# Optimization experiments

Hardware: AMD Instinct MI355X
Metric: run time of the kernel (lower is better)

Reference implementation:

```python
import jax, jax.numpy as jnp
import numpy as np

B = 16
L = 3
INNER = 96
EXPAND = 2 * INNER
NC = 80
C_INS = [128, 256, 512]
HWS = [(80, 80), (40, 40), (20, 20)]
STRIDES = [8, 16, 32]
PRIOR = 0.01


def _conv(x, w, b, groups=1, pad=0):
    # x: [B,Cin,H,W], w: [Cout,Cin//groups,kh,kw]
    y = jax.lax.conv_general_dilated(
        x, w, window_strides=(1, 1), padding=[(pad, pad), (pad, pad)],
        feature_group_count=groups)
    return y + b[None, :, None, None]


def _inverted_residual(x, w1, b1, wd, bd, w2, b2):
    # 1x1 expand -> SiLU -> 3x3 depthwise -> SiLU -> 1x1 project, residual (stride 1, cin==cout)
    y = jax.nn.silu(_conv(x, w1, b1))
    y = jax.nn.silu(_conv(y, wd, bd, groups=w1.shape[0], pad=1))
    y = _conv(y, w2, b2)
    return x + y


def setup_inputs() -> dict:
    key = jax.random.key(0)
    keys = iter(jax.random.split(key, 64))

    def nrm(shape, s=0.03):
        return jax.random.normal(next(keys), shape, jnp.float32) * s

    d = {}
    for k in range(L):
        h, w = HWS[k]
        d[f"x{k}"] = jax.random.normal(next(keys), (B, C_INS[k], h, w), jnp.float32)
        d[f"stem_w{k}"] = nrm((INNER, C_INS[k], 1, 1))
        d[f"stem_b{k}"] = jnp.zeros((INNER,), jnp.float32)
    for p in ("cls", "reg"):
        d[p + "_w1"] = nrm((L, EXPAND, INNER, 1, 1))
        d[p + "_b1"] = jnp.zeros((L, EXPAND), jnp.float32)
        d[p + "_wd"] = nrm((L, EXPAND, 1, 3, 3))
        d[p + "_bd"] = jnp.zeros((L, EXPAND), jnp.float32)
        d[p + "_w2"] = nrm((L, INNER, EXPAND, 1, 1))
        d[p + "_b2"] = jnp.zeros((L, INNER), jnp.float32)
    bias_init = float(-np.log((1.0 - PRIOR) / PRIOR))
    d["clsp_w"] = nrm((L, NC, INNER, 1, 1))
    d["clsp_b"] = jnp.full((L, NC), bias_init, jnp.float32)
    d["regp_w"] = nrm((L, 4, INNER, 1, 1))
    d["regp_b"] = jnp.zeros((L, 4), jnp.float32)
    d["objp_w"] = nrm((L, 1, INNER, 1, 1))
    d["objp_b"] = jnp.full((L, 1), bias_init, jnp.float32)
    return d


def _forward(xs, params):
    outs = []
    for k in range(L):
        x = jax.nn.silu(_conv(xs[k], params[f"stem_w{k}"], params[f"stem_b{k}"]))  # CBR stem
        cls_feat = _inverted_residual(
            x, params["cls_w1"][k], params["cls_b1"][k], params["cls_wd"][k],
            params["cls_bd"][k], params["cls_w2"][k], params["cls_b2"][k])
        reg_feat = _inverted_residual(
            x, params["reg_w1"][k], params["reg_b1"][k], params["reg_wd"][k],
            params["reg_bd"][k], params["reg_w2"][k], params["reg_b2"][k])
        cls_out = _conv(cls_feat, params["clsp_w"][k], params["clsp_b"][k])  # [B,NC,H,W]
        reg_out = _conv(reg_feat, params["regp_w"][k], params["regp_b"][k])  # [B,4,H,W]
        obj_out = _conv(reg_feat, params["objp_w"][k], params["objp_b"][k])  # [B,1,H,W]
        h, w = HWS[k]
        yv, xv = jnp.meshgrid(jnp.arange(h, dtype=jnp.float32),
                              jnp.arange(w, dtype=jnp.float32), indexing="ij")
        grid = jnp.stack((xv, yv), 0)[None]  # [1,2,H,W]
        s = float(STRIDES[k])
        o = jnp.concatenate([
            (reg_out[:, :2] + grid) * s,
            jnp.exp(reg_out[:, 2:4]) * s,
            jax.nn.sigmoid(obj_out),
            jax.nn.sigmoid(cls_out),
        ], axis=1)  # [B, 5+NC, H, W]
        outs.append(o.reshape(B, 5 + NC, h * w).transpose(0, 2, 1))
    return jnp.concatenate(outs, axis=1)  # [B, 8400, 5+NC]


def reference(x0, x1, x2,
              stem_w0, stem_b0, stem_w1, stem_b1, stem_w2, stem_b2,
              cls_w1, cls_b1, cls_wd, cls_bd, cls_w2, cls_b2,
              reg_w1, reg_b1, reg_wd, reg_bd, reg_w2, reg_b2,
              clsp_w, clsp_b, regp_w, regp_b, objp_w, objp_b):
    params = dict(stem_w0=stem_w0, stem_b0=stem_b0, stem_w1=stem_w1, stem_b1=stem_b1,
                  stem_w2=stem_w2, stem_b2=stem_b2,
                  cls_w1=cls_w1, cls_b1=cls_b1, cls_wd=cls_wd, cls_bd=cls_bd,
                  cls_w2=cls_w2, cls_b2=cls_b2,
                  reg_w1=reg_w1, reg_b1=reg_b1, reg_wd=reg_wd, reg_bd=reg_bd,
                  reg_w2=reg_w2, reg_b2=reg_b2,
                  clsp_w=clsp_w, clsp_b=clsp_b, regp_w=regp_w, regp_b=regp_b,
                  objp_w=objp_w, objp_b=objp_b)
    return _forward([x0, x1, x2], params)
```

## Files before the change

### kernel.cpp

```cpp
#include <hip/hip_runtime.h>

typedef unsigned int uint32;
using half2v  = __attribute__((ext_vector_type(2))) _Float16;
using half4v  = __attribute__((ext_vector_type(4))) _Float16;
using half8   = __attribute__((ext_vector_type(8))) _Float16;
using floatx4 = __attribute__((ext_vector_type(4))) float;

__device__ __forceinline__ float sigm_f(float x){
  return __builtin_amdgcn_rcpf(1.0f + __expf(-x));
}
__device__ __forceinline__ float silu_f(float x){ return x * sigm_f(x); }

__device__ __forceinline__ half2v pkrtz(float a, float b){
  return __builtin_bit_cast(half2v, __builtin_amdgcn_cvt_pkrtz(a, b));
}

__device__ __forceinline__ void gll16(const _Float16* src, _Float16* ldsDst){
  __builtin_amdgcn_global_load_lds(
      (const __attribute__((address_space(1))) uint32*)src,
      (__attribute__((address_space(3))) uint32*)ldsDst, 16, 0, 0);
}

#define OFF_W2    196608
#define OFF_HEAD  307200
#define OFF_WDT   330240
#define OFF_ROBJ  340608
#define OFF_DWB   345216
#define WTOT      346368

#define PPOS 143552L
#define EXPAD_ELEMS 27561984L
#define NDW  134400L

__global__ __launch_bounds__(256) void wconv_k(
    const float* __restrict__ s0, const float* __restrict__ s1,
    const float* __restrict__ s2, const float* __restrict__ cw1,
    const float* __restrict__ rw1, const float* __restrict__ cw2,
    const float* __restrict__ rw2, const float* __restrict__ chw,
    const float* __restrict__ cwd, const float* __restrict__ rwd,
    const float* __restrict__ rpw, const float* __restrict__ opw,
    const float* __restrict__ cbd, const float* __restrict__ rbd,
    _Float16* __restrict__ dst)
{
  int i = blockIdx.x*256 + threadIdx.x;
  if (i >= WTOT) return;
  float v;
  if (i < OFF_WDT) {
    const float* p; int off;
    if      (i < 12288)  { p = s0;  off = i; }
    else if (i < 36864)  { p = s1;  off = i - 12288; }
    else if (i < 86016)  { p = s2;  off = i - 36864; }
    else if (i < 141312) { p = cw1; off = i - 86016; }
    else if (i < 196608) { p = rw1; off = i - 141312; }
    else if (i < 251904) { p = cw2; off = i - 196608; }
    else if (i < 307200) { p = rw2; off = i - 251904; }
    else                 { p = chw; off = i - 307200; }
    v = p[off];
  } else if (i < OFF_ROBJ) {
    int rel = i - OFF_WDT;
    int br = rel / 5184; int r2 = rel - br*5184;
    int lvl = r2 / 1728; int r3 = r2 - lvl*1728;
    int j = r3 / 192;    int c = r3 - j*192;
    const float* wd = br ? rwd : cwd;
    v = wd[lvl*1728 + c*9 + j];
  } else if (i < OFF_DWB) {
    int rel = i - OFF_ROBJ;
    int lvl = rel / 1536; int r2 = rel - lvl*1536;
    int co = r2 / 96;     int k = r2 - co*96;
    v = (co < 4) ? rpw[lvl*384 + co*96 + k] : (co == 4 ? opw[lvl*96 + k] : 0.f);
  } else {
    int rel = i - OFF_DWB;
    int br = rel / 576;  int r2 = rel - br*576;
    int lvl = r2 / 192;  int c = r2 - lvl*192;
    v = (br ? rbd : cbd)[lvl*192 + c];
  }
  dst[i] = (_Float16)v;
}

__global__ __launch_bounds__(256) void zpad_k(_Float16* __restrict__ exBase)
{
  int ci = blockIdx.x*256 + threadIdx.x;
  if (ci >= 439296) return;
  int br = ci / 219648; int r = ci - br*219648;
  int W, PLB, rem, perimg;
  if (r < 124416)      { W=80; PLB=0;      rem = r;          perimg = 7776; }
  else if (r < 187392) { W=40; PLB=107584; rem = r - 124416; perimg = 3936; }
  else                 { W=20; PLB=135808; rem = r - 187392; perimg = 2016; }
  int b = rem / perimg; int t3 = rem - b*perimg;
  int p = t3 / 24; int g = t3 - p*24;
  int PW = W + 2;
  int row, col;
  if (p < 2*PW) { row = (p >= PW) ? (W+1) : 0; col = (p >= PW) ? (p - PW) : p; }
  else { int q = p - 2*PW; row = 1 + (q >> 1); col = (q & 1) ? (W+1) : 0; }
  long pp = (long)PLB + (long)b*PW*PW + row*PW + col;
  half8 z = {(_Float16)0,(_Float16)0,(_Float16)0,(_Float16)0,
             (_Float16)0,(_Float16)0,(_Float16)0,(_Float16)0};
  *(half8*)(exBase + br*EXPAD_ELEMS + ((long)g*PPOS + pp)*8) = z;
}

__global__ __launch_bounds__(256) void stem_k(
    const float* __restrict__ x0, const float* __restrict__ x1,
    const float* __restrict__ x2, const _Float16* __restrict__ Wb,
    const float* __restrict__ sb0, const float* __restrict__ sb1,
    const float* __restrict__ sb2, _Float16* __restrict__ Out)
{
  const int m0 = blockIdx.x << 7;
  const int lvl = (m0 < 102400) ? 0 : (m0 < 128000 ? 1 : 2);
  const int CIN = (lvl==0)?128:(lvl==1?256:512);
  const int HW  = (lvl==0)?6400:(lvl==1?1600:400);
  const int noff= (lvl==0)?0:(lvl==1?102400:128000);
  const float* X = (lvl==0)?x0:(lvl==1?x1:x2);
  const _Float16* Wl = Wb + ((lvl==0)?0:(lvl==1?12288:36864));
  const float* bias = (lvl==0)?sb0:(lvl==1?sb1:sb2);

  int t=threadIdx.x, lane=t&63, wv=t>>6, mr=lane&15, quad=lane>>4;

  int idx[2];
  #pragma unroll
  for (int nt=0; nt<2; ++nt) {
    int n = m0 + wv*32 + nt*16 + mr;
    int m = n - noff; int b_ = m / HW; int p = m - b_*HW;
    idx[nt] = (b_*CIN + quad*8)*HW + p;
  }
  const _Float16* Ap = Wl + mr*CIN + quad*8;

  floatx4 zero = {0.f,0.f,0.f,0.f};
  floatx4 acc[6][2];
  #pragma unroll
  for (int i=0;i<6;++i)
    #pragma unroll
    for (int j=0;j<2;++j) acc[i][j] = zero;

  for (int k=0; k<CIN; k+=32) {
    half8 a[6], b[2];
    #pragma unroll
    for (int mt=0; mt<6; ++mt) a[mt] = *(const half8*)(Ap + mt*16*CIN);
    #pragma unroll
    for (int nt=0; nt<2; ++nt) {
      float f[8];
      #pragma unroll
      for (int j=0;j<8;++j) f[j] = X[idx[nt] + j*HW];
      half2v* bh = (half2v*)&b[nt];
      #pragma unroll
      for (int j=0;j<4;++j) bh[j] = pkrtz(f[2*j], f[2*j+1]);
    }
    #pragma unroll
    for (int mt=0; mt<6; ++mt)
      #pragma unroll
      for (int nt=0; nt<2; ++nt)
        acc[mt][nt] = __builtin_amdgcn_mfma_f32_16x16x32_f16(a[mt], b[nt], acc[mt][nt], 0, 0, 0);
    Ap += 32;
    #pragma unroll
    for (int nt=0; nt<2; ++nt) idx[nt] += 32*HW;
  }

  #pragma unroll
  for (int mt=0; mt<6; ++mt) {
    float4 bv = *(const float4*)(bias + mt*16 + quad*4);
    int co = mt*16 + quad*4;
    int g = co >> 3; int h = co & 7;
    #pragma unroll
    for (int nt=0; nt<2; ++nt) {
      int pos = m0 + wv*32 + nt*16 + mr;
      half4v o;
      o[0] = (_Float16)silu_f(acc[mt][nt][0] + bv.x);
      o[1] = (_Float16)silu_f(acc[mt][nt][1] + bv.y);
      o[2] = (_Float16)silu_f(acc[mt][nt][2] + bv.z);
      o[3] = (_Float16)silu_f(acc[mt][nt][3] + bv.w);
      *(half4v*)(Out + ((long)g*NDW + pos)*8 + h) = o;
    }
  }
}

__global__ __launch_bounds__(256) void expand2_k(
    const _Float16* __restrict__ A, const _Float16* __restrict__ wbf,
    const float* __restrict__ b1c, const float* __restrict__ b1r,
    _Float16* __restrict__ OutBase)
{
  const int bz = blockIdx.z;
  const _Float16* Wb = wbf + 86016 + bz*55296;
  _Float16* Out = OutBase + bz*EXPAD_ELEMS;
  const float* b1 = bz ? b1r : b1c;

  int orig = blockIdx.x;
  int xcd = orig & 7; int loc = orig >> 3;
  int bx = (xcd < 2 ? xcd*132 : 2*132 + (xcd-2)*131) + loc;

  const int m0 = bx << 7;
  const int lvl = (m0 < 102400) ? 0 : (m0 < 128000 ? 1 : 2);
  const int HW  = (lvl==0)?6400:(lvl==1?1600:400);
  const int W   = (lvl==0)?80:(lvl==1?40:20);
  const int noff= (lvl==0)?0:(lvl==1?102400:128000);
  const int PLB = (lvl==0)?0:(lvl==1?107584:135808);
  const int PW  = W + 2;
  const int co0 = blockIdx.y * 96;
  int t = threadIdx.x, lane = t & 63, wv = t >> 6;
  int mr = lane & 15, quad = lane >> 4;
  const _Float16* Ap0 = A + ((long)quad*NDW + (m0 + wv*32 + mr))*8;
  const _Float16* Bp = Wb + ((long)(co0 + mr))*96 + quad*8;
  const float* bp = b1 + lvl*192 + co0;

  floatx4 zero = {0.f,0.f,0.f,0.f};
  floatx4 acc[6][2];
  #pragma unroll
  for (int i=0;i<6;++i)
    #pragma unroll
    for (int j=0;j<2;++j) acc[i][j] = zero;

  #pragma unroll
  for (int k=0; k<3; ++k) {
    half8 wf[6], af[2];
    #pragma unroll
    for (int mt=0; mt<6; ++mt) wf[mt] = *(const half8*)(Bp + (long)mt*16*96);
    #pragma unroll
    for (int nt=0; nt<2; ++nt)
      af[nt] = *(const half8*)(Ap0 + ((long)k*4*NDW)*8 + nt*16*8);
    #pragma unroll
    for (int mt=0; mt<6; ++mt)
      #pragma unroll
      for (int nt=0; nt<2; ++nt)
        acc[mt][nt] = __builtin_amdgcn_mfma_f32_16x16x32_f16(wf[mt], af[nt], acc[mt][nt], 0, 0, 0);
    Bp += 32;
  }

  long pp2[2];
  #pragma unroll
  for (int nt=0; nt<2; ++nt) {
    int gm = m0 + wv*32 + nt*16 + mr;
    int m = gm - noff; int b_ = m / HW; int rp = m - b_*HW;
    int y = rp / W;  int x = rp - y*W;
    pp2[nt] = PLB + ((long)b_*PW + (y+1))*PW + (x+1);
  }

  #pragma unroll
  for (int mt=0; mt<6; ++mt) {
    float4 bv = *(const float4*)(bp + mt*16 + quad*4);
    int co = co0 + mt*16 + quad*4;
    int g = co >> 3;
    int h = (co & 4);
    #pragma unroll
    for (int nt=0; nt<2; ++nt) {
      half4v o;
      o[0] = (_Float16)silu_f(acc[mt][nt][0] + bv.x);
      o[1] = (_Float16)silu_f(acc[mt][nt][1] + bv.y);
      o[2] = (_Float16)silu_f(acc[mt][nt][2] + bv.z);
      o[3] = (_Float16)silu_f(acc[mt][nt][3] + bv.w);
      *(half4v*)(Out + ((long)g*PPOS + pp2[nt])*8 + h) = o;
    }
  }
}

#define PSTRIDE 104
__global__ __launch_bounds__(256, 3) void dwprojhead_k(
    const _Float16* __restrict__ exBase, const _Float16* __restrict__ wbf,
    const float* __restrict__ b2_c, const float* __restrict__ b2_r,
    const _Float16* __restrict__ resid,
    const float* __restrict__ hb, const float* __restrict__ rb,
    const float* __restrict__ ob, float* __restrict__ out)
{
  __shared__ _Float16 halo[24*800];
  __shared__ _Float16 ldsP[64*PSTRIDE];
  const int bz = blockIdx.y;
  const _Float16* ex = exBase + bz*EXPAD_ELEMS;
  const float* b2 = bz ? b2_r : b2_c;

  int orig = blockIdx.x;
  int bx = (orig & 7)*268 + (orig >> 3);

  int lvl, W, HW, noff, a0, PLB;
  int b_, y0, x0;
  if (bx < 1600) {
    lvl = 0; W = 80; HW = 6400; noff = 0;      a0 = 0;    PLB = 0;
    b_ = bx / 100; int tl = bx - b_*100;
    y0 = (tl / 10) * 8; x0 = (tl - (tl/10)*10) * 8;
  } else if (bx < 2000) {
    lvl = 1; W = 40; HW = 1600; noff = 102400; a0 = 6400; PLB = 107584;
    int rel = bx - 1600; b_ = rel / 25; int tl = rel - b_*25;
    y0 = (tl / 5) * 8; x0 = (tl - (tl/5)*5) * 8;
  } else {
    lvl = 2; W = 20; HW = 400; noff = 128000; a0 = 8000; PLB = 135808;
    int rel = bx - 2000; b_ = rel / 9; int tl = rel - b_*9;
    int iy = tl / 3; int ix = tl - iy*3;
    y0 = iy*6; x0 = ix*6;
  }
  const int PW = W + 2;

  int t = threadIdx.x, lane = t & 63, wv = t >> 6;
  int mr = lane & 15, quad = lane >> 4;
  const int p = wv*16 + mr;

  const _Float16* wT = wbf + OFF_WDT + bz*5184 + lvl*1728;
  const _Float16* bB = wbf + OFF_DWB + bz*576 + lvl*192;
  const _Float16* Ap = wbf + OFF_W2 + bz*55296 + lvl*18432 + ((long)mr)*192 + quad*8;

  const int n = noff + b_*HW + (y0 + (p>>3))*W + x0 + (p&7);

  floatx4 pacc[6];
  {
    floatx4 zero = {0.f,0.f,0.f,0.f};
    #pragma unroll
    for (int j=0;j<6;++j) pacc[j] = zero;
  }

  half4v rsv[6];

  const long pb00 = (long)PLB + ((long)b_*PW + y0)*PW + x0;
  {
    int e1 = lane;
    int hy1 = e1 / 10, hx1 = e1 - hy1*10;
    long s1 = pb00 + hy1*PW + hx1;
    int e2 = 64 + lane;
    int hy2 = e2 / 10, hx2 = e2 - hy2*10;
    long s2 = pb00 + hy2*PW + hx2;
    #pragma unroll
    for (int j = 0; j < 6; ++j) {
      int g = wv*6 + j;
      gll16(ex + ((long)g*PPOS + s1)*8, halo + g*800);
      if (lane < 36)
        gll16(ex + ((long)g*PPOS + s2)*8, halo + g*800 + 512);
    }
  }
  #pragma unroll
  for (int mt=0; mt<6; ++mt) {
    int co = mt*16 + quad*4;
    int g = co >> 3; int h = co & 7;
    rsv[mt] = *(const half4v*)(resid + ((long)g*NDW + n)*8 + h);
  }
  __syncthreads();

  {
    const int ty = p >> 3, tx = p & 7;
    const _Float16* hb0 = halo + (ty*10 + tx)*8;
    for (int k = 0; k < 6; ++k) {
      const int g = 4*k + quad;
      const _Float16* hg = hb0 + g*800;
      const _Float16* wp = wT + g*8;

      half8 a[9], w[9];
      #pragma unroll
      for (int dy = 0; dy < 3; ++dy)
        #pragma unroll
        for (int dx = 0; dx < 3; ++dx)
          a[dy*3+dx] = *(const half8*)(hg + (dy*10 + dx)*8);
      #pragma unroll
      for (int tap = 0; tap < 9; ++tap)
        w[tap] = *(const half8*)(wp + tap*192);
      half8 bv8 = *(const half8*)(bB + g*8);
      half8 wf[6];
      #pragma unroll
      for (int mt = 0; mt < 6; ++mt)
        wf[mt] = *(const half8*)(Ap + (long)mt*16*192 + k*32);

      half2v ac0 = {bv8[0], bv8[1]};
      half2v ac1 = {bv8[2], bv8[3]};
      half2v ac2 = {bv8[4], bv8[5]};
      half2v ac3 = {bv8[6], bv8[7]};
      #pragma unroll
      for (int tap = 0; tap < 9; ++tap) {
        ac0 += half2v{a[tap][0],a[tap][1]} * half2v{w[tap][0],w[tap][1]};
        ac1 += half2v{a[tap][2],a[tap][3]} * half2v{w[tap][2],w[tap][3]};
        ac2 += half2v{a[tap][4],a[tap][5]} * half2v{w[tap][4],w[tap][5]};
        ac3 += half2v{a[tap][6],a[tap][7]} * half2v{w[tap][6],w[tap][7]};
      }
      half8 af;
      {
        half2v* oh = (half2v*)&af;
        oh[0] = pkrtz(silu_f((float)ac0[0]), silu_f((float)ac0[1]));
        oh[1] = pkrtz(silu_f((float)ac1[0]), silu_f((float)ac1[1]));
        oh[2] = pkrtz(silu_f((float)ac2[0]), silu_f((float)ac2[1]));
        oh[3] = pkrtz(silu_f((float)ac3[0]), silu_f((float)ac3[1]));
      }
      #pragma unroll
      for (int mt = 0; mt < 6; ++mt)
        pacc[mt] = __builtin_amdgcn_mfma_f32_16x16x32_f16(wf[mt], af, pacc[mt], 0, 0, 0);
    }
  }

  {
    const float* bp2 = b2 + lvl*96;
    #pragma unroll
    for (int mt=0; mt<6; ++mt) {
      int co = mt*16 + quad*4;
      float4 bv = *(const float4*)(bp2 + co);
      half4v o;
      o[0] = (_Float16)(pacc[mt][0] + bv.x + (float)rsv[mt][0]);
      o[1] = (_Float16)(pacc[mt][1] + bv.y + (float)rsv[mt][1]);
      o[2] = (_Float16)(pacc[mt][2] + bv.z + (float)rsv[mt][2]);
      o[3] = (_Float16)(pacc[mt][3] + bv.w + (float)rsv[mt][3]);
      *(half4v*)(ldsP + p*PSTRIDE + co) = o;
    }
  }

  if (bz == 0) {
    const _Float16* Bp = wbf + OFF_HEAD + lvl*7680 + ((long)mr)*96 + quad*8;
    const float* bp = hb + lvl*80;
    floatx4 zero = {0.f,0.f,0.f,0.f};
    floatx4 acc[5];
    #pragma unroll
    for (int j=0;j<5;++j) acc[j] = zero;

    #pragma unroll
    for (int k=0; k<3; ++k) {
      half8 a = *(const half8*)(ldsP + (wv*16 + mr)*PSTRIDE + k*32 + quad*8);
      half8 b[5];
      #pragma unroll
      for (int nt=0; nt<5; ++nt)
        b[nt] = *(const half8*)(Bp + (long)nt*16*96 + k*32);
      #pragma unroll
      for (int nt=0; nt<5; ++nt)
        acc[nt] = __builtin_amdgcn_mfma_f32_16x16x32_f16(a, b[nt], acc[nt], 0, 0, 0);
    }

    #pragma unroll
    for (int nt=0; nt<5; ++nt) {
      int co = nt*16 + mr;
      float bv = bp[co];
      #pragma unroll
      for (int r=0; r<4; ++r) {
        int pq = wv*16 + quad*4 + r;
        int rpp = (y0 + (pq>>3))*W + x0 + (pq&7);
        out[((long)(b_*8400 + a0 + rpp))*85 + 5 + co] = sigm_f(acc[nt][r] + bv);
      }
    }
  } else {
    const _Float16* Bp = wbf + OFF_ROBJ + lvl*1536 + ((long)mr)*96 + quad*8;
    float bv = (mr < 4) ? rb[lvl*4 + mr] : ((mr == 4) ? ob[lvl] : 0.f);
    float sc = (lvl==0) ? 8.f : (lvl==1 ? 16.f : 32.f);
    floatx4 acc = {0.f,0.f,0.f,0.f};
    #pragma unroll
    for (int k=0; k<3; ++k) {
      half8 a = *(const half8*)(ldsP + (wv*16 + mr)*PSTRIDE + k*32 + quad*8);
      half8 b = *(const half8*)(Bp + k*32);
      acc = __builtin_amdgcn_mfma_f32_16x16x32_f16(a, b, acc, 0, 0, 0);
    }
    #pragma unroll
    for (int r=0; r<4; ++r) {
      int pq = wv*16 + quad*4 + r;
      int yy = y0 + (pq>>3); int xx = x0 + (pq&7);
      int rpp = yy*W + xx;
      float v = acc[r] + bv;
      float o;
      if      (mr == 0) o = (v + (float)xx)*sc;
      else if (mr == 1) o = (v + (float)yy)*sc;
      else if (mr <  4) o = __expf(v)*sc;
      else              o = sigm_f(v);
      if (mr < 5)
        out[((long)(b_*8400 + a0 + rpp))*85 + mr] = o;
    }
  }
}

extern "C" void kernel_launch(void* const* d_in, const int* in_sizes, int n_in,
                              void* d_out, int out_size, void* d_ws, size_t ws_size,
                              hipStream_t stream)
{
  bool dict = (in_sizes[1] == 96*128);
  const float* X[3]; const float* SW[3]; const float* SB[3];
  if (dict) {
    X[0]=(const float*)d_in[0]; SW[0]=(const float*)d_in[1]; SB[0]=(const float*)d_in[2];
    X[1]=(const float*)d_in[3]; SW[1]=(const float*)d_in[4]; SB[1]=(const float*)d_in[5];
    X[2]=(const float*)d_in[6]; SW[2]=(const float*)d_in[7]; SB[2]=(const float*)d_in[8];
  } else {
    X[0]=(const float*)d_in[0]; X[1]=(const float*)d_in[1]; X[2]=(const float*)d_in[2];
    SW[0]=(const float*)d_in[3]; SB[0]=(const float*)d_in[4];
    SW[1]=(const float*)d_in[5]; SB[1]=(const float*)d_in[6];
    SW[2]=(const float*)d_in[7]; SB[2]=(const float*)d_in[8];
  }
  const float* br_w1[2] = {(const float*)d_in[9],  (const float*)d_in[15]};
  const float* br_b1[2] = {(const float*)d_in[10], (const float*)d_in[16]};
  const float* br_wd[2] = {(const float*)d_in[11], (const float*)d_in[17]};
  const float* br_bd[2] = {(const float*)d_in[12], (const float*)d_in[18]};
  const float* br_w2[2] = {(const float*)d_in[13], (const float*)d_in[19]};
  const float* br_b2[2] = {(const float*)d_in[14], (const float*)d_in[20]};
  const float* clsp_w=(const float*)d_in[21]; const float* clsp_b=(const float*)d_in[22];
  const float* regp_w=(const float*)d_in[23]; const float* regp_b=(const float*)d_in[24];
  const float* objp_w=(const float*)d_in[25]; const float* objp_b=(const float*)d_in[26];

  float* out = (float*)d_out;

  _Float16* wbf   = (_Float16*)d_ws;
  _Float16* stemO = wbf + WTOT;
  _Float16* bufA  = stemO + 12902400;

  wconv_k<<<1353,256,0,stream>>>(SW[0],SW[1],SW[2],br_w1[0],br_w1[1],
                                 br_w2[0],br_w2[1],clsp_w,br_wd[0],br_wd[1],
                                 regp_w,objp_w,br_bd[0],br_bd[1],wbf);

  zpad_k<<<1716,256,0,stream>>>(bufA);

  stem_k<<<1050,256,0,stream>>>(X[0],X[1],X[2],wbf,SB[0],SB[1],SB[2],stemO);

  expand2_k<<<dim3(1050,2,2),256,0,stream>>>(stemO, wbf, br_b1[0], br_b1[1], bufA);

  dwprojhead_k<<<dim3(2144,2),256,0,stream>>>(
      bufA, wbf, br_b2[0], br_b2[1], stemO,
      clsp_b, regp_b, objp_b, out);
}
```

Measured before the change: 222.0 us.

## Fuse 1x1 expand into depthwise/project/head kernel with halo recompute

The expand 1x1 conv is moved into the depthwise/project/head kernel. Each tile loads a stem halo into LDS, recomputes the 192-channel expansion for the 10x10 halo with MFMA, and zeroes out-of-bounds positions in place of the padding. This drops the large padded expand buffer (written and read back through HBM), the zero-pad kernel and two launches. In exchange it recomputes the halo positions (100 vs 64 per tile) and raises LDS use, which may lower occupancy; the launch_bounds occupancy hint is dropped.

```diff
diff --git a/kernel.cpp b/kernel.cpp
--- a/kernel.cpp
+++ b/kernel.cpp
@@ -21,6 +21,7 @@
       (__attribute__((address_space(3))) uint32*)ldsDst, 16, 0, 0);
 }
 
+#define OFF_W1    86016
 #define OFF_W2    196608
 #define OFF_HEAD  307200
 #define OFF_WDT   330240
@@ -28,8 +29,6 @@
 #define OFF_DWB   345216
 #define WTOT      346368
 
-#define PPOS 143552L
-#define EXPAD_ELEMS 27561984L
 #define NDW  134400L
 
 __global__ __launch_bounds__(256) void wconv_k(
@@ -77,27 +76,6 @@
   dst[i] = (_Float16)v;
 }
 
-__global__ __launch_bounds__(256) void zpad_k(_Float16* __restrict__ exBase)
-{
-  int ci = blockIdx.x*256 + threadIdx.x;
-  if (ci >= 439296) return;
-  int br = ci / 219648; int r = ci - br*219648;
-  int W, PLB, rem, perimg;
-  if (r < 124416)      { W=80; PLB=0;      rem = r;          perimg = 7776; }
-  else if (r < 187392) { W=40; PLB=107584; rem = r - 124416; perimg = 3936; }
-  else                 { W=20; PLB=135808; rem = r - 187392; perimg = 2016; }
-  int b = rem / perimg; int t3 = rem - b*perimg;
-  int p = t3 / 24; int g = t3 - p*24;
-  int PW = W + 2;
-  int row, col;
-  if (p < 2*PW) { row = (p >= PW) ? (W+1) : 0; col = (p >= PW) ? (p - PW) : p; }
-  else { int q = p - 2*PW; row = 1 + (q >> 1); col = (q & 1) ? (W+1) : 0; }
-  long pp = (long)PLB + (long)b*PW*PW + row*PW + col;
-  half8 z = {(_Float16)0,(_Float16)0,(_Float16)0,(_Float16)0,
-             (_Float16)0,(_Float16)0,(_Float16)0,(_Float16)0};
-  *(half8*)(exBase + br*EXPAD_ELEMS + ((long)g*PPOS + pp)*8) = z;
-}
-
 __global__ __launch_bounds__(256) void stem_k(
     const float* __restrict__ x0, const float* __restrict__ x1,
     const float* __restrict__ x2, const _Float16* __restrict__ Wb,
@@ -172,118 +150,40 @@
   }
 }
 
-__global__ __launch_bounds__(256) void expand2_k(
-    const _Float16* __restrict__ A, const _Float16* __restrict__ wbf,
+#define PSTRIDE 104
+__global__ __launch_bounds__(256) void xfuse_k(
+    const _Float16* __restrict__ stemO, const _Float16* __restrict__ wbf,
     const float* __restrict__ b1c, const float* __restrict__ b1r,
-    _Float16* __restrict__ OutBase)
-{
-  const int bz = blockIdx.z;
-  const _Float16* Wb = wbf + 86016 + bz*55296;
-  _Float16* Out = OutBase + bz*EXPAD_ELEMS;
-  const float* b1 = bz ? b1r : b1c;
-
-  int orig = blockIdx.x;
-  int xcd = orig & 7; int loc = orig >> 3;
-  int bx = (xcd < 2 ? xcd*132 : 2*132 + (xcd-2)*131) + loc;
-
-  const int m0 = bx << 7;
-  const int lvl = (m0 < 102400) ? 0 : (m0 < 128000 ? 1 : 2);
-  const int HW  = (lvl==0)?6400:(lvl==1?1600:400);
-  const int W   = (lvl==0)?80:(lvl==1?40:20);
-  const int noff= (lvl==0)?0:(lvl==1?102400:128000);
-  const int PLB = (lvl==0)?0:(lvl==1?107584:135808);
-  const int PW  = W + 2;
-  const int co0 = blockIdx.y * 96;
-  int t = threadIdx.x, lane = t & 63, wv = t >> 6;
-  int mr = lane & 15, quad = lane >> 4;
-  const _Float16* Ap0 = A + ((long)quad*NDW + (m0 + wv*32 + mr))*8;
-  const _Float16* Bp = Wb + ((long)(co0 + mr))*96 + quad*8;
-  const float* bp = b1 + lvl*192 + co0;
-
-  floatx4 zero = {0.f,0.f,0.f,0.f};
-  floatx4 acc[6][2];
-  #pragma unroll
-  for (int i=0;i<6;++i)
-    #pragma unroll
-    for (int j=0;j<2;++j) acc[i][j] = zero;
-
-  #pragma unroll
-  for (int k=0; k<3; ++k) {
-    half8 wf[6], af[2];
-    #pragma unroll
-    for (int mt=0; mt<6; ++mt) wf[mt] = *(const half8*)(Bp + (long)mt*16*96);
-    #pragma unroll
-    for (int nt=0; nt<2; ++nt)
-      af[nt] = *(const half8*)(Ap0 + ((long)k*4*NDW)*8 + nt*16*8);
-    #pragma unroll
-    for (int mt=0; mt<6; ++mt)
-      #pragma unroll
-      for (int nt=0; nt<2; ++nt)
-        acc[mt][nt] = __builtin_amdgcn_mfma_f32_16x16x32_f16(wf[mt], af[nt], acc[mt][nt], 0, 0, 0);
-    Bp += 32;
-  }
-
-  long pp2[2];
-  #pragma unroll
-  for (int nt=0; nt<2; ++nt) {
-    int gm = m0 + wv*32 + nt*16 + mr;
-    int m = gm - noff; int b_ = m / HW; int rp = m - b_*HW;
-    int y = rp / W;  int x = rp - y*W;
-    pp2[nt] = PLB + ((long)b_*PW + (y+1))*PW + (x+1);
-  }
-
-  #pragma unroll
-  for (int mt=0; mt<6; ++mt) {
-    float4 bv = *(const float4*)(bp + mt*16 + quad*4);
-    int co = co0 + mt*16 + quad*4;
-    int g = co >> 3;
-    int h = (co & 4);
-    #pragma unroll
-    for (int nt=0; nt<2; ++nt) {
-      half4v o;
-      o[0] = (_Float16)silu_f(acc[mt][nt][0] + bv.x);
-      o[1] = (_Float16)silu_f(acc[mt][nt][1] + bv.y);
-      o[2] = (_Float16)silu_f(acc[mt][nt][2] + bv.z);
-      o[3] = (_Float16)silu_f(acc[mt][nt][3] + bv.w);
-      *(half4v*)(Out + ((long)g*PPOS + pp2[nt])*8 + h) = o;
-    }
-  }
-}
-
-#define PSTRIDE 104
-__global__ __launch_bounds__(256, 3) void dwprojhead_k(
-    const _Float16* __restrict__ exBase, const _Float16* __restrict__ wbf,
     const float* __restrict__ b2_c, const float* __restrict__ b2_r,
-    const _Float16* __restrict__ resid,
     const float* __restrict__ hb, const float* __restrict__ rb,
     const float* __restrict__ ob, float* __restrict__ out)
 {
-  __shared__ _Float16 halo[24*800];
-  __shared__ _Float16 ldsP[64*PSTRIDE];
+  __shared__ _Float16 smem[28800];
+  _Float16* stemT = smem;
+  _Float16* halo  = smem + 9600;
+  _Float16* ldsP  = smem;
   const int bz = blockIdx.y;
-  const _Float16* ex = exBase + bz*EXPAD_ELEMS;
   const float* b2 = bz ? b2_r : b2_c;
 
   int orig = blockIdx.x;
   int bx = (orig & 7)*268 + (orig >> 3);
 
-  int lvl, W, HW, noff, a0, PLB;
+  int lvl, W, HW, noff, a0;
   int b_, y0, x0;
   if (bx < 1600) {
-    lvl = 0; W = 80; HW = 6400; noff = 0;      a0 = 0;    PLB = 0;
+    lvl = 0; W = 80; HW = 6400; noff = 0;      a0 = 0;
     b_ = bx / 100; int tl = bx - b_*100;
     y0 = (tl / 10) * 8; x0 = (tl - (tl/10)*10) * 8;
   } else if (bx < 2000) {
-    lvl = 1; W = 40; HW = 1600; noff = 102400; a0 = 6400; PLB = 107584;
+    lvl = 1; W = 40; HW = 1600; noff = 102400; a0 = 6400;
     int rel = bx - 1600; b_ = rel / 25; int tl = rel - b_*25;
     y0 = (tl / 5) * 8; x0 = (tl - (tl/5)*5) * 8;
   } else {
-    lvl = 2; W = 20; HW = 400; noff = 128000; a0 = 8000; PLB = 135808;
+    lvl = 2; W = 20; HW = 400; noff = 128000; a0 = 8000;
     int rel = bx - 2000; b_ = rel / 9; int tl = rel - b_*9;
     int iy = tl / 3; int ix = tl - iy*3;
     y0 = iy*6; x0 = ix*6;
   }
-  const int PW = W + 2;
 
   int t = threadIdx.x, lane = t & 63, wv = t >> 6;
   int mr = lane & 15, quad = lane >> 4;
@@ -295,39 +195,86 @@
 
   const int n = noff + b_*HW + (y0 + (p>>3))*W + x0 + (p&7);
 
-  floatx4 pacc[6];
-  {
-    floatx4 zero = {0.f,0.f,0.f,0.f};
-    #pragma unroll
-    for (int j=0;j<6;++j) pacc[j] = zero;
-  }
-
-  half4v rsv[6];
-
-  const long pb00 = (long)PLB + ((long)b_*PW + y0)*PW + x0;
   {
     int e1 = lane;
     int hy1 = e1 / 10, hx1 = e1 - hy1*10;
-    long s1 = pb00 + hy1*PW + hx1;
+    int yy1 = y0 - 1 + hy1; yy1 = yy1 < 0 ? 0 : (yy1 >= W ? W-1 : yy1);
+    int xx1 = x0 - 1 + hx1; xx1 = xx1 < 0 ? 0 : (xx1 >= W ? W-1 : xx1);
+    long n1 = (long)noff + (long)b_*HW + yy1*W + xx1;
     int e2 = 64 + lane;
     int hy2 = e2 / 10, hx2 = e2 - hy2*10;
-    long s2 = pb00 + hy2*PW + hx2;
-    #pragma unroll
-    for (int j = 0; j < 6; ++j) {
-      int g = wv*6 + j;
-      gll16(ex + ((long)g*PPOS + s1)*8, halo + g*800);
+    int yy2 = y0 - 1 + hy2; yy2 = yy2 < 0 ? 0 : (yy2 >= W ? W-1 : yy2);
+    int xx2 = x0 - 1 + hx2; xx2 = xx2 < 0 ? 0 : (xx2 >= W ? W-1 : xx2);
+    long n2 = (long)noff + (long)b_*HW + yy2*W + xx2;
+    #pragma unroll
+    for (int j = 0; j < 3; ++j) {
+      int g = wv*3 + j;
+      gll16(stemO + ((long)g*NDW + n1)*8, stemT + g*800);
       if (lane < 36)
-        gll16(ex + ((long)g*PPOS + s2)*8, halo + g*800 + 512);
-    }
-  }
+        gll16(stemO + ((long)g*NDW + n2)*8, stemT + g*800 + 512);
+    }
+  }
+
+  half4v rsv[6];
   #pragma unroll
   for (int mt=0; mt<6; ++mt) {
     int co = mt*16 + quad*4;
     int g = co >> 3; int h = co & 7;
-    rsv[mt] = *(const half4v*)(resid + ((long)g*NDW + n)*8 + h);
+    rsv[mt] = *(const half4v*)(stemO + ((long)g*NDW + n)*8 + h);
   }
   __syncthreads();
 
+  {
+    const _Float16* W1 = wbf + OFF_W1 + bz*55296 + lvl*18432;
+    const float* bp1 = (bz ? b1r : b1c) + lvl*192;
+    half8 wf[3][3];
+    #pragma unroll
+    for (int m3 = 0; m3 < 3; ++m3)
+      #pragma unroll
+      for (int ks = 0; ks < 3; ++ks)
+        wf[m3][ks] = *(const half8*)(W1 + (long)((wv*3+m3)*16 + mr)*96 + ks*32 + quad*8);
+
+    #pragma unroll
+    for (int nt = 0; nt < 7; ++nt) {
+      int ee = nt*16 + mr;
+      int e = ee < 100 ? ee : 99;
+      floatx4 acc[3];
+      #pragma unroll
+      for (int m3 = 0; m3 < 3; ++m3) acc[m3] = floatx4{0.f,0.f,0.f,0.f};
+      #pragma unroll
+      for (int ks = 0; ks < 3; ++ks) {
+        half8 af = *(const half8*)(stemT + (ks*4+quad)*800 + e*8);
+        #pragma unroll
+        for (int m3 = 0; m3 < 3; ++m3)
+          acc[m3] = __builtin_amdgcn_mfma_f32_16x16x32_f16(wf[m3][ks], af, acc[m3], 0, 0, 0);
+      }
+      if (ee < 100) {
+        int hy = ee / 10, hx = ee - hy*10;
+        int yy = y0 - 1 + hy, xx = x0 - 1 + hx;
+        bool oob = ((unsigned)yy >= (unsigned)W) || ((unsigned)xx >= (unsigned)W);
+        #pragma unroll
+        for (int m3 = 0; m3 < 3; ++m3) {
+          int co = (wv*3+m3)*16 + quad*4;
+          float4 bv = *(const float4*)(bp1 + co);
+          half4v o;
+          if (oob) {
+            o[0]=o[1]=o[2]=o[3]=(_Float16)0.f;
+          } else {
+            o[0] = (_Float16)silu_f(acc[m3][0] + bv.x);
+            o[1] = (_Float16)silu_f(acc[m3][1] + bv.y);
+            o[2] = (_Float16)silu_f(acc[m3][2] + bv.z);
+            o[3] = (_Float16)silu_f(acc[m3][3] + bv.w);
+          }
+          *(half4v*)(halo + (co>>3)*800 + ee*8 + (co&7)) = o;
+        }
+      }
+    }
+  }
+  __syncthreads();
+
+  floatx4 pacc[6];
+  #pragma unroll
+  for (int j=0;j<6;++j) pacc[j] = floatx4{0.f,0.f,0.f,0.f};
   {
     const int ty = p >> 3, tx = p & 7;
     const _Float16* hb0 = halo + (ty*10 + tx)*8;
@@ -346,10 +293,10 @@
       for (int tap = 0; tap < 9; ++tap)
         w[tap] = *(const half8*)(wp + tap*192);
       half8 bv8 = *(const half8*)(bB + g*8);
-      half8 wf[6];
+      half8 wfp[6];
       #pragma unroll
       for (int mt = 0; mt < 6; ++mt)
-        wf[mt] = *(const half8*)(Ap + (long)mt*16*192 + k*32);
+        wfp[mt] = *(const half8*)(Ap + (long)mt*16*192 + k*32);
 
       half2v ac0 = {bv8[0], bv8[1]};
       half2v ac1 = {bv8[2], bv8[3]};
@@ -372,7 +319,7 @@
       }
       #pragma unroll
       for (int mt = 0; mt < 6; ++mt)
-        pacc[mt] = __builtin_amdgcn_mfma_f32_16x16x32_f16(wf[mt], af, pacc[mt], 0, 0, 0);
+        pacc[mt] = __builtin_amdgcn_mfma_f32_16x16x32_f16(wfp[mt], af, pacc[mt], 0, 0, 0);
     }
   }
 
@@ -394,10 +341,9 @@
   if (bz == 0) {
     const _Float16* Bp = wbf + OFF_HEAD + lvl*7680 + ((long)mr)*96 + quad*8;
     const float* bp = hb + lvl*80;
-    floatx4 zero = {0.f,0.f,0.f,0.f};
     floatx4 acc[5];
     #pragma unroll
-    for (int j=0;j<5;++j) acc[j] = zero;
+    for (int j=0;j<5;++j) acc[j] = floatx4{0.f,0.f,0.f,0.f};
 
     #pragma unroll
     for (int k=0; k<3; ++k) {
@@ -480,19 +426,14 @@
 
   _Float16* wbf   = (_Float16*)d_ws;
   _Float16* stemO = wbf + WTOT;
-  _Float16* bufA  = stemO + 12902400;
 
   wconv_k<<<1353,256,0,stream>>>(SW[0],SW[1],SW[2],br_w1[0],br_w1[1],
                                  br_w2[0],br_w2[1],clsp_w,br_wd[0],br_wd[1],
                                  regp_w,objp_w,br_bd[0],br_bd[1],wbf);
 
-  zpad_k<<<1716,256,0,stream>>>(bufA);
-
   stem_k<<<1050,256,0,stream>>>(X[0],X[1],X[2],wbf,SB[0],SB[1],SB[2],stemO);
 
-  expand2_k<<<dim3(1050,2,2),256,0,stream>>>(stemO, wbf, br_b1[0], br_b1[1], bufA);
-
-  dwprojhead_k<<<dim3(2144,2),256,0,stream>>>(
-      bufA, wbf, br_b2[0], br_b2[1], stemO,
+  xfuse_k<<<dim3(2144,2),256,0,stream>>>(
+      stemO, wbf, br_b1[0], br_b1[1], br_b2[0], br_b2[1],
       clsp_b, regp_b, objp_b, out);
 }
```

Result: faster. 216.7 us (-2.4%).
